# Performance work log

Hardware: AMD Instinct MI355X
Metric: run time of the kernel (lower is better)

Reference implementation:

```python
import jax, jax.numpy as jnp
import numpy as np

N, E = 100000, 640000
IN, H, C, L = 128, 128, 64, 5
BN_EPS = 1e-5


def setup_inputs() -> dict:
    key = jax.random.key(0)
    ks = jax.random.split(key, 12)
    x = jax.random.normal(ks[0], (N, IN), jnp.float32)
    edge_index = jax.random.randint(ks[1], (2, E), 0, N, dtype=jnp.int64)
    # GCNConv weights: layer0 in->hidden, layers 1..4 hidden->hidden
    W_in = jax.random.normal(ks[2], (IN, H), jnp.float32) / np.sqrt(IN).astype(np.float32)
    b_in = jnp.zeros((H,), jnp.float32)
    Ws = jax.random.normal(ks[3], (L - 1, H, H), jnp.float32) / np.sqrt(H).astype(np.float32)
    bs = jnp.zeros((L - 1, H), jnp.float32)
    # BatchNorm1d (eval mode) params per layer
    gammas = jnp.ones((L, H), jnp.float32)
    betas = jnp.zeros((L, H), jnp.float32)
    run_mean = 0.1 * jax.random.normal(ks[4], (L, H), jnp.float32)
    run_var = jax.random.uniform(ks[5], (L, H), jnp.float32) + 0.5
    # final node-level classifier
    W_out = jax.random.normal(ks[6], (H, C), jnp.float32) / np.sqrt(H).astype(np.float32)
    b_out = jnp.zeros((C,), jnp.float32)
    return {"x": x, "edge_index": edge_index, "W_in": W_in, "b_in": b_in,
            "Ws": Ws, "bs": bs, "gammas": gammas, "betas": betas,
            "run_mean": run_mean, "run_var": run_var, "W_out": W_out, "b_out": b_out}


def reference(x, edge_index, W_in, b_in, Ws, bs, gammas, betas, run_mean, run_var, W_out, b_out):
    src, dst = edge_index[0], edge_index[1]
    n = x.shape[0]
    # GCN symmetric norm with self-loops: deg counts incoming edges + 1
    deg = jax.ops.segment_sum(jnp.ones(src.shape, x.dtype), dst, num_segments=n) + 1.0
    dis = jax.lax.rsqrt(deg)                      # deg^{-1/2}, [N]
    coef = dis[src] * dis[dst]                    # per-edge norm, [E]
    self_coef = (dis * dis)[:, None]              # self-loop norm deg^{-1}, [N,1]

    h = x
    for l in range(L):
        W = W_in if l == 0 else Ws[l - 1]
        b = b_in if l == 0 else bs[l - 1]
        t = h @ W                                 # [N,H]
        agg = jax.ops.segment_sum(t[src] * coef[:, None], dst, num_segments=n)
        agg = agg + t * self_coef + b             # neighbor agg + self loop + bias
        # BatchNorm1d in eval mode (running stats)
        y = (agg - run_mean[l]) * jax.lax.rsqrt(run_var[l] + BN_EPS) * gammas[l] + betas[l]
        h = jax.nn.relu(y)                        # dropout is identity in eval
    return h @ W_out + b_out                      # [N, num_classes]
```

## Files before the change

### kernel.cpp

```cpp
#include <hip/hip_runtime.h>
#include <cstdint>

#define BN_EPS 1e-5f

typedef __bf16 bf16x8 __attribute__((ext_vector_type(8)));
typedef __bf16 bf16x4 __attribute__((ext_vector_type(4)));
typedef __bf16 bf16x2 __attribute__((ext_vector_type(2)));
typedef float f32x4 __attribute__((ext_vector_type(4)));


__global__ __launch_bounds__(256) void k_count(const int* __restrict__ dstv,
                                               int* __restrict__ counts,
                                               int* __restrict__ rank, int E) {
  int e = blockIdx.x * 256 + threadIdx.x;
  if (e < E) rank[e] = atomicAdd(counts + dstv[e], 1);
}

__global__ __launch_bounds__(256) void k_dis(const int* __restrict__ counts,
                                             float* __restrict__ dis, int N) {
  int i = blockIdx.x * 256 + threadIdx.x;
  if (i < N) dis[i] = rsqrtf((float)counts[i] + 1.0f);
}

__global__ __launch_bounds__(256) void k_scan1(const int* __restrict__ counts,
                                               int* __restrict__ rowstart,
                                               int* __restrict__ bsum, int N) {
  __shared__ int wsum[4];
  const int tid = threadIdx.x, lane = tid & 63, wv = tid >> 6;
  const int base = blockIdx.x * 1024 + tid * 4;
  int c[4];
#pragma unroll
  for (int j = 0; j < 4; ++j) {
    int idx = base + j;
    c[j] = (idx < N) ? counts[idx] : 0;
  }
  int s = c[0] + c[1] + c[2] + c[3];
  int x = s;
  for (int d = 1; d < 64; d <<= 1) {
    int y = __shfl_up(x, d);
    if (lane >= d) x += y;
  }
  if (lane == 63) wsum[wv] = x;
  __syncthreads();
  int woff = 0;
  for (int w = 0; w < wv; ++w) woff += wsum[w];
  int r = woff + x - s;
#pragma unroll
  for (int j = 0; j < 4; ++j) {
    int idx = base + j;
    if (idx < N) rowstart[idx] = r;
    r += c[j];
  }
  if (tid == 255) bsum[blockIdx.x] = woff + x;
}

__global__ __launch_bounds__(256) void k_scan2(const int* __restrict__ bsum,
                                               int* __restrict__ boff, int nb) {
  __shared__ int sm[256];
  const int tid = threadIdx.x;
  int v = (tid < nb) ? bsum[tid] : 0;
  sm[tid] = v;
  __syncthreads();
  for (int d = 1; d < 256; d <<= 1) {
    int y = (tid >= d) ? sm[tid - d] : 0;
    __syncthreads();
    sm[tid] += y;
    __syncthreads();
  }
  if (tid < nb) boff[tid] = sm[tid] - v;
}

__global__ __launch_bounds__(256) void k_fix(int* __restrict__ rowstart,
                                             const int* __restrict__ boff, int N) {
  int i = blockIdx.x * 256 + threadIdx.x;
  if (i < N) rowstart[i] += boff[i >> 10];
}

__global__ __launch_bounds__(256) void k_scatter(const int* __restrict__ src,
                                                 const int* __restrict__ dstv,
                                                 const int* __restrict__ rowstart,
                                                 const int* __restrict__ rank,
                                                 int* __restrict__ esrc, int E) {
  int e = blockIdx.x * 256 + threadIdx.x;
  if (e < E) esrc[rowstart[dstv[e]] + rank[e]] = src[e];
}

__global__ __launch_bounds__(256) void k_bnparam(const float* __restrict__ gamma,
                                                 const float* __restrict__ beta,
                                                 const float* __restrict__ mean,
                                                 const float* __restrict__ var,
                                                 float* __restrict__ scale,
                                                 float* __restrict__ shift, int n) {
  int i = blockIdx.x * 256 + threadIdx.x;
  if (i < n) {
    float s = gamma[i] * rsqrtf(var[i] + BN_EPS);
    scale[i] = s;
    shift[i] = beta[i] - mean[i] * s;
  }
}

__global__ __launch_bounds__(64) void k_zrow(__bf16* __restrict__ t, int N) {
  bf16x2 z;
  z[0] = (__bf16)0.f;
  z[1] = (__bf16)0.f;
  *reinterpret_cast<bf16x2*>(t + (size_t)N * 128 + threadIdx.x * 2) = z;
}

__global__ __launch_bounds__(256) void k_wprep(const float* __restrict__ W_in,
                                               const float* __restrict__ Ws,
                                               const float* __restrict__ W_out,
                                               __bf16* __restrict__ wfrag) {
  const int idx = blockIdx.x * 256 + threadIdx.x;
  if (idx >= 11264) return;
  int l, r, CT;
  if (idx < 10240) { l = idx >> 11; r = idx & 2047; CT = 8; }
  else             { l = 5; r = idx - 10240; CT = 4; }
  const int lane = r & 63;
  const int rr = r >> 6;
  const int ct = rr % CT;
  const int kc_i = rr / CT;
  const int lr = lane & 15, kg = lane >> 4;
  const int col = ct * 16 + lr;
  const int k0 = kc_i * 32 + kg * 8;
  const float* Wsrc;
  int ncols;
  if (l == 0)      { Wsrc = W_in; ncols = 128; }
  else if (l <= 4) { Wsrc = Ws + (size_t)(l - 1) * 16384; ncols = 128; }
  else             { Wsrc = W_out; ncols = 64; }
  bf16x8 hi, lo;
#pragma unroll
  for (int j = 0; j < 8; ++j) {
    float v = Wsrc[(size_t)(k0 + j) * ncols + col];
    __bf16 h = (__bf16)v;
    hi[j] = h;
    lo[j] = (__bf16)(v - (float)h);
  }
  const size_t lbase = (l < 5) ? (size_t)l * 65536 : (size_t)327680;
  char* outp = (char*)wfrag + lbase;
  *(bf16x8*)(outp + ((size_t)(kc_i * 2 + 0) * CT + ct) * 1024 + lane * 16) = hi;
  *(bf16x8*)(outp + ((size_t)(kc_i * 2 + 1) * CT + ct) * 1024 + lane * 16) = lo;
}

__global__ __launch_bounds__(256, 4) void k_mgemm0(
    const float* __restrict__ in, const __bf16* __restrict__ wfrag,
    const float* __restrict__ dis, __bf16* __restrict__ outh, int N) {
  constexpr int CT = 8;
  __shared__ __align__(16) char Abase[32768];

  const int tid = threadIdx.x;
  const int lane = tid & 63;
  const int wv = tid >> 6;
  const int lr = lane & 15;
  const int kg = lane >> 4;
  const int rowBase = blockIdx.x * 128;

  {
    const int kq = tid & 31;
#pragma unroll
    for (int i = 0; i < 16; ++i) {
      const int row = (tid >> 5) + i * 8;
      const int grow = rowBase + row;
      float4 v = make_float4(0.f, 0.f, 0.f, 0.f);
      if (grow < N) v = *(const float4*)(in + (size_t)grow * 128 + kq * 4);
      bf16x4 h;
      h[0] = (__bf16)v.x; h[1] = (__bf16)v.y; h[2] = (__bf16)v.z; h[3] = (__bf16)v.w;
      int byte = row * 256 + kq * 8;
      byte ^= (row & 7) << 4;
      *(bf16x4*)(Abase + byte) = h;
    }
  }
  __syncthreads();

  f32x4 acc[2][CT] = {};
#pragma unroll
  for (int kc_i = 0; kc_i < 4; ++kc_i) {
    bf16x8 afr[2];
#pragma unroll
    for (int rt = 0; rt < 2; ++rt) {
      const int row = wv * 32 + rt * 16 + lr;
      int byte = row * 256 + kc_i * 64 + kg * 16;
      byte ^= (row & 7) << 4;
      afr[rt] = *(const bf16x8*)(Abase + byte);
    }
    const char* wk = (const char*)wfrag + (size_t)kc_i * (2 * CT * 1024) +
                     (size_t)lane * 16;
#pragma unroll
    for (int ct = 0; ct < CT; ++ct) {
      bf16x8 bhi = *(const bf16x8*)(wk + ct * 1024);
      bf16x8 blo = *(const bf16x8*)(wk + (CT + ct) * 1024);
#pragma unroll
      for (int rt = 0; rt < 2; ++rt) {
        acc[rt][ct] = __builtin_amdgcn_mfma_f32_16x16x32_bf16(afr[rt], bhi,
                                                              acc[rt][ct], 0, 0, 0);
        acc[rt][ct] = __builtin_amdgcn_mfma_f32_16x16x32_bf16(afr[rt], blo,
                                                              acc[rt][ct], 0, 0, 0);
      }
    }
  }

#pragma unroll
  for (int rt = 0; rt < 2; ++rt) {
#pragma unroll
    for (int j = 0; j < 4; ++j) {
      const int row = rowBase + wv * 32 + rt * 16 + kg * 4 + j;
      if (row < N) {
        const float dr = dis[row];
#pragma unroll
        for (int ct = 0; ct < CT; ++ct)
          outh[(size_t)row * 128 + ct * 16 + lr] = (__bf16)(acc[rt][ct][j] * dr);
      }
    }
  }
}

template <int CT, bool FINAL>
__global__ __launch_bounds__(256, 4) void k_layer(
    const __bf16* __restrict__ tin, const __bf16* __restrict__ wfrag,
    const int* __restrict__ rowstart, const int* __restrict__ counts,
    const int* __restrict__ esrc, const float* __restrict__ dis,
    const float* __restrict__ bias, const float* __restrict__ scale,
    const float* __restrict__ shift, const float* __restrict__ out_bias,
    float* __restrict__ outf, __bf16* __restrict__ outh, int N) {
  __shared__ __align__(16) char Abase[32768];

  const int tid = threadIdx.x;
  const int lane = tid & 63;
  const int wv = tid >> 6;
  const int lr = lane & 15;
  const int kg = lane >> 4;
  const int rowBase = blockIdx.x * 128;

  {
    const int nb0 = rowBase + wv * 32;
    int mb = 0, mc = 0, mdbits = 0;
    if (lane < 32) {
      const int nd = nb0 + lane;
      if (nd < N) {
        mb = rowstart[nd];
        mc = counts[nd];
        mdbits = __float_as_int(dis[nd]);
      }
    }
    const int f0 = lane * 2;
    const float bx = bias[f0], by = bias[f0 + 1];
    const float scx = scale[f0], scy = scale[f0 + 1];
    const float shx = shift[f0], shy = shift[f0 + 1];

    int ci = __builtin_amdgcn_readlane(mc, 0);
    int rec = (lane < ci) ? esrc[__builtin_amdgcn_readlane(mb, 0) + lane] : N;

    for (int i = 0; i < 32; ++i) {
      const int node = nb0 + i;
      const float dn = __int_as_float(__builtin_amdgcn_readlane(mdbits, i));
      const int srow = (node < N) ? node : N;
      const bf16x2 sv =
          *reinterpret_cast<const bf16x2*>(tin + (size_t)srow * 128 + f0);
      int rec_n = N, cn = 0;
      if (i < 31) {
        const int bn_ = __builtin_amdgcn_readlane(mb, i + 1);
        cn = __builtin_amdgcn_readlane(mc, i + 1);
        if (lane < cn) rec_n = esrc[bn_ + lane];
      }
      float ax = (float)sv[0];
      float ay = (float)sv[1];
      const int m = ci < 64 ? ci : 64;
      const int rounds = (m + 7) >> 3;
      for (int r = 0; r < rounds; ++r) {
        const int rb = r * 8;
#pragma unroll
        for (int u = 0; u < 8; ++u) {
          const int s = __builtin_amdgcn_readlane(rec, rb + u);
          const bf16x2 v =
              *reinterpret_cast<const bf16x2*>(tin + (size_t)s * 128 + f0);
          ax += (float)v[0];
          ay += (float)v[1];
        }
      }
      if (__builtin_expect(ci > 64, 0)) {
        const int bi = __builtin_amdgcn_readlane(mb, i);
        for (int e = 64; e < ci; ++e) {
          const int s0 = esrc[bi + e];
          const bf16x2 v0 =
              *reinterpret_cast<const bf16x2*>(tin + (size_t)s0 * 128 + f0);
          ax += (float)v0[0];
          ay += (float)v0[1];
        }
      }
      ax = fmaf(ax, dn, bx);
      ay = fmaf(ay, dn, by);
      ax = fmaxf(fmaf(ax, scx, shx), 0.f);
      ay = fmaxf(fmaf(ay, scy, shy), 0.f);
      bf16x2 o;
      o[0] = (__bf16)ax;
      o[1] = (__bf16)ay;
      const int row = wv * 32 + i;
      int byte = row * 256 + lane * 4;
      byte ^= (row & 7) << 4;
      *(bf16x2*)(Abase + byte) = o;
      rec = rec_n;
      ci = cn;
    }
  }
  __syncthreads();

  f32x4 acc[2][CT] = {};
#pragma unroll
  for (int kc_i = 0; kc_i < 4; ++kc_i) {
    bf16x8 afr[2];
#pragma unroll
    for (int rt = 0; rt < 2; ++rt) {
      const int row = wv * 32 + rt * 16 + lr;
      int byte = row * 256 + kc_i * 64 + kg * 16;
      byte ^= (row & 7) << 4;
      afr[rt] = *(const bf16x8*)(Abase + byte);
    }
    const char* wk = (const char*)wfrag + (size_t)kc_i * (2 * CT * 1024) +
                     (size_t)lane * 16;
#pragma unroll
    for (int ct = 0; ct < CT; ++ct) {
      bf16x8 bhi = *(const bf16x8*)(wk + ct * 1024);
      bf16x8 blo = *(const bf16x8*)(wk + (CT + ct) * 1024);
#pragma unroll
      for (int rt = 0; rt < 2; ++rt) {
        acc[rt][ct] = __builtin_amdgcn_mfma_f32_16x16x32_bf16(afr[rt], bhi,
                                                              acc[rt][ct], 0, 0, 0);
        acc[rt][ct] = __builtin_amdgcn_mfma_f32_16x16x32_bf16(afr[rt], blo,
                                                              acc[rt][ct], 0, 0, 0);
      }
    }
  }

  float ob[CT];
  if constexpr (FINAL) {
#pragma unroll
    for (int ct = 0; ct < CT; ++ct) ob[ct] = out_bias[ct * 16 + lr];
  }
#pragma unroll
  for (int rt = 0; rt < 2; ++rt) {
#pragma unroll
    for (int j = 0; j < 4; ++j) {
      const int row = rowBase + wv * 32 + rt * 16 + kg * 4 + j;
      if (row < N) {
        if constexpr (FINAL) {
#pragma unroll
          for (int ct = 0; ct < CT; ++ct)
            outf[(size_t)row * (CT * 16) + ct * 16 + lr] = acc[rt][ct][j] + ob[ct];
        } else {
          const float dr = dis[row];
#pragma unroll
          for (int ct = 0; ct < CT; ++ct)
            outh[(size_t)row * 128 + ct * 16 + lr] = (__bf16)(acc[rt][ct][j] * dr);
        }
      }
    }
  }
}

extern "C" void kernel_launch(void* const* d_in, const int* in_sizes, int n_in,
                              void* d_out, int out_size, void* d_ws, size_t ws_size,
                              hipStream_t stream) {
  const float* x      = (const float*)d_in[0];
  const int*   ei     = (const int*)d_in[1];
  const float* W_in   = (const float*)d_in[2];
  const float* b_in   = (const float*)d_in[3];
  const float* Ws     = (const float*)d_in[4];
  const float* bs     = (const float*)d_in[5];
  const float* gammas = (const float*)d_in[6];
  const float* betas  = (const float*)d_in[7];
  const float* mean   = (const float*)d_in[8];
  const float* var    = (const float*)d_in[9];
  const float* W_out  = (const float*)d_in[10];
  const float* b_out  = (const float*)d_in[11];
  float* out = (float*)d_out;

  const int N = in_sizes[0] / 128;
  const int E = in_sizes[1] / 2;
  const int* src = ei;
  const int* dst = ei + E;

  char* ws = (char*)d_ws;
  size_t off = 0;
  auto alloc = [&](size_t bytes) {
    void* p = ws + off;
    off = (off + bytes + 255) & ~255ULL;
    return p;
  };
  int*    counts   = (int*)alloc((size_t)N * 4);
  int*    rowstart = (int*)alloc((size_t)N * 4);
  int*    bsum     = (int*)alloc(256 * 4);
  int*    boff     = (int*)alloc(256 * 4);
  float*  dis      = (float*)alloc((size_t)N * 4);
  float*  scale    = (float*)alloc(5 * 128 * 4);
  float*  shift    = (float*)alloc(5 * 128 * 4);
  __bf16* wfrag    = (__bf16*)alloc(360448);
  int*    rank     = (int*)alloc((size_t)E * 4);
  int*    esrc     = (int*)alloc((size_t)E * 4);
  __bf16* tA       = (__bf16*)alloc(((size_t)N + 1) * 128 * 2);
  __bf16* tB       = (__bf16*)alloc(((size_t)N + 1) * 128 * 2);
  (void)ws_size;

  const int nb = (N + 1023) / 1024;

  hipMemsetAsync(counts, 0, (size_t)N * 4, stream);
  k_count<<<(E + 255) / 256, 256, 0, stream>>>(dst, counts, rank, E);
  k_dis<<<(N + 255) / 256, 256, 0, stream>>>(counts, dis, N);
  k_scan1<<<nb, 256, 0, stream>>>(counts, rowstart, bsum, N);
  k_scan2<<<1, 256, 0, stream>>>(bsum, boff, nb);
  k_fix<<<(N + 255) / 256, 256, 0, stream>>>(rowstart, boff, N);
  k_scatter<<<(E + 255) / 256, 256, 0, stream>>>(src, dst, rowstart, rank, esrc, E);
  k_bnparam<<<(5 * 128 + 255) / 256, 256, 0, stream>>>(gammas, betas, mean, var,
                                                       scale, shift, 5 * 128);
  k_wprep<<<44, 256, 0, stream>>>(W_in, Ws, W_out, wfrag);
  k_zrow<<<1, 64, 0, stream>>>(tA, N);
  k_zrow<<<1, 64, 0, stream>>>(tB, N);

  const int gblocks = (N + 127) / 128;

  k_mgemm0<<<gblocks, 256, 0, stream>>>(x, wfrag, dis, tA, N);

  const float* biases[5] = {b_in, bs, bs + 128, bs + 256, bs + 384};
  __bf16* tin = tA;
  __bf16* tout = tB;
  for (int l = 1; l <= 4; ++l) {
    k_layer<8, false><<<gblocks, 256, 0, stream>>>(
        tin, wfrag + (size_t)l * 32768, rowstart, counts, esrc, dis,
        biases[l - 1], scale + (l - 1) * 128, shift + (l - 1) * 128, nullptr,
        nullptr, tout, N);
    __bf16* tmp = tin;
    tin = tout;
    tout = tmp;
  }
  k_layer<4, true><<<gblocks, 256, 0, stream>>>(
      tin, wfrag + 163840, rowstart, counts, esrc, dis, biases[4],
      scale + 4 * 128, shift + 4 * 128, b_out, out, nullptr, N);
}
```

Before: 334.5 us.

## Halve layer tile to 64 rows per block and drop block barrier

The fused aggregate+GEMM layer kernel now handles 64 rows per block, so each wave gathers and multiplies only its own 16 rows. Shared memory per block is halved and launch bounds are raised to allow more resident blocks. The __syncthreads is replaced by a block-scope fence because each wave reads back only the LDS rows it wrote itself. The aim is more waves in flight to hide the latency of the irregular neighbor gathers, at the cost of twice as many blocks, less reuse of each weight fragment load across rows, and tighter register limits.

```diff
diff --git a/kernel.cpp b/kernel.cpp
--- a/kernel.cpp
+++ b/kernel.cpp
@@ -214,26 +214,26 @@
 }
 
 template <int CT, bool FINAL>
-__global__ __launch_bounds__(256, 4) void k_layer(
+__global__ __launch_bounds__(256, 6) void k_layer(
     const __bf16* __restrict__ tin, const __bf16* __restrict__ wfrag,
     const int* __restrict__ rowstart, const int* __restrict__ counts,
     const int* __restrict__ esrc, const float* __restrict__ dis,
     const float* __restrict__ bias, const float* __restrict__ scale,
     const float* __restrict__ shift, const float* __restrict__ out_bias,
     float* __restrict__ outf, __bf16* __restrict__ outh, int N) {
-  __shared__ __align__(16) char Abase[32768];
+  __shared__ __align__(16) char Abase[16384];
 
   const int tid = threadIdx.x;
   const int lane = tid & 63;
   const int wv = tid >> 6;
   const int lr = lane & 15;
   const int kg = lane >> 4;
-  const int rowBase = blockIdx.x * 128;
+  const int rowBase = blockIdx.x * 64;
 
   {
-    const int nb0 = rowBase + wv * 32;
+    const int nb0 = rowBase + wv * 16;
     int mb = 0, mc = 0, mdbits = 0;
-    if (lane < 32) {
+    if (lane < 16) {
       const int nd = nb0 + lane;
       if (nd < N) {
         mb = rowstart[nd];
@@ -249,14 +249,14 @@
     int ci = __builtin_amdgcn_readlane(mc, 0);
     int rec = (lane < ci) ? esrc[__builtin_amdgcn_readlane(mb, 0) + lane] : N;
 
-    for (int i = 0; i < 32; ++i) {
+    for (int i = 0; i < 16; ++i) {
       const int node = nb0 + i;
       const float dn = __int_as_float(__builtin_amdgcn_readlane(mdbits, i));
       const int srow = (node < N) ? node : N;
       const bf16x2 sv =
           *reinterpret_cast<const bf16x2*>(tin + (size_t)srow * 128 + f0);
       int rec_n = N, cn = 0;
-      if (i < 31) {
+      if (i < 15) {
         const int bn_ = __builtin_amdgcn_readlane(mb, i + 1);
         cn = __builtin_amdgcn_readlane(mc, i + 1);
         if (lane < cn) rec_n = esrc[bn_ + lane];
@@ -293,7 +293,7 @@
       bf16x2 o;
       o[0] = (__bf16)ax;
       o[1] = (__bf16)ay;
-      const int row = wv * 32 + i;
+      const int row = wv * 16 + i;
       int byte = row * 256 + lane * 4;
       byte ^= (row & 7) << 4;
       *(bf16x2*)(Abase + byte) = o;
@@ -301,32 +301,23 @@
       ci = cn;
     }
   }
-  __syncthreads();
-
-  f32x4 acc[2][CT] = {};
+  __threadfence_block();
+
+  f32x4 acc[CT] = {};
 #pragma unroll
   for (int kc_i = 0; kc_i < 4; ++kc_i) {
-    bf16x8 afr[2];
-#pragma unroll
-    for (int rt = 0; rt < 2; ++rt) {
-      const int row = wv * 32 + rt * 16 + lr;
-      int byte = row * 256 + kc_i * 64 + kg * 16;
-      byte ^= (row & 7) << 4;
-      afr[rt] = *(const bf16x8*)(Abase + byte);
-    }
+    const int row = wv * 16 + lr;
+    int byte = row * 256 + kc_i * 64 + kg * 16;
+    byte ^= (row & 7) << 4;
+    const bf16x8 afr = *(const bf16x8*)(Abase + byte);
     const char* wk = (const char*)wfrag + (size_t)kc_i * (2 * CT * 1024) +
                      (size_t)lane * 16;
 #pragma unroll
     for (int ct = 0; ct < CT; ++ct) {
       bf16x8 bhi = *(const bf16x8*)(wk + ct * 1024);
       bf16x8 blo = *(const bf16x8*)(wk + (CT + ct) * 1024);
-#pragma unroll
-      for (int rt = 0; rt < 2; ++rt) {
-        acc[rt][ct] = __builtin_amdgcn_mfma_f32_16x16x32_bf16(afr[rt], bhi,
-                                                              acc[rt][ct], 0, 0, 0);
-        acc[rt][ct] = __builtin_amdgcn_mfma_f32_16x16x32_bf16(afr[rt], blo,
-                                                              acc[rt][ct], 0, 0, 0);
-      }
+      acc[ct] = __builtin_amdgcn_mfma_f32_16x16x32_bf16(afr, bhi, acc[ct], 0, 0, 0);
+      acc[ct] = __builtin_amdgcn_mfma_f32_16x16x32_bf16(afr, blo, acc[ct], 0, 0, 0);
     }
   }
 
@@ -336,21 +327,18 @@
     for (int ct = 0; ct < CT; ++ct) ob[ct] = out_bias[ct * 16 + lr];
   }
 #pragma unroll
-  for (int rt = 0; rt < 2; ++rt) {
-#pragma unroll
-    for (int j = 0; j < 4; ++j) {
-      const int row = rowBase + wv * 32 + rt * 16 + kg * 4 + j;
-      if (row < N) {
-        if constexpr (FINAL) {
-#pragma unroll
-          for (int ct = 0; ct < CT; ++ct)
-            outf[(size_t)row * (CT * 16) + ct * 16 + lr] = acc[rt][ct][j] + ob[ct];
-        } else {
-          const float dr = dis[row];
-#pragma unroll
-          for (int ct = 0; ct < CT; ++ct)
-            outh[(size_t)row * 128 + ct * 16 + lr] = (__bf16)(acc[rt][ct][j] * dr);
-        }
+  for (int j = 0; j < 4; ++j) {
+    const int row = rowBase + wv * 16 + kg * 4 + j;
+    if (row < N) {
+      if constexpr (FINAL) {
+#pragma unroll
+        for (int ct = 0; ct < CT; ++ct)
+          outf[(size_t)row * (CT * 16) + ct * 16 + lr] = acc[ct][j] + ob[ct];
+      } else {
+        const float dr = dis[row];
+#pragma unroll
+        for (int ct = 0; ct < CT; ++ct)
+          outh[(size_t)row * 128 + ct * 16 + lr] = (__bf16)(acc[ct][j] * dr);
       }
     }
   }
@@ -415,6 +403,7 @@
   k_zrow<<<1, 64, 0, stream>>>(tB, N);
 
   const int gblocks = (N + 127) / 128;
+  const int lblocks = (N + 63) / 64;
 
   k_mgemm0<<<gblocks, 256, 0, stream>>>(x, wfrag, dis, tA, N);
 
@@ -422,7 +411,7 @@
   __bf16* tin = tA;
   __bf16* tout = tB;
   for (int l = 1; l <= 4; ++l) {
-    k_layer<8, false><<<gblocks, 256, 0, stream>>>(
+    k_layer<8, false><<<lblocks, 256, 0, stream>>>(
         tin, wfrag + (size_t)l * 32768, rowstart, counts, esrc, dis,
         biases[l - 1], scale + (l - 1) * 128, shift + (l - 1) * 128, nullptr,
         nullptr, tout, N);
@@ -430,7 +419,7 @@
     tin = tout;
     tout = tmp;
   }
-  k_layer<4, true><<<gblocks, 256, 0, stream>>>(
+  k_layer<4, true><<<lblocks, 256, 0, stream>>>(
       tin, wfrag + 163840, rowstart, counts, esrc, dis, biases[4],
       scale + 4 * 128, shift + 4 * 128, b_out, out, nullptr, N);
 }
```

New measurement: 293.4 us. 12.3% less time.
